# Performance work log

Hardware: AMD Instinct MI355X
Metric: run time of the kernel (lower is better)

The kernel has to match this reference:

```python
import jax, jax.numpy as jnp
import numpy as np

B, L, DM = 2, 1024, 1024
DI = 2 * DM          # expand=2
N = 16               # d_state
K = 4                # d_conv
DTR = DM // 16       # dt_rank = ceil(d_model/16) = 64
EPS = 1e-5


def setup_inputs() -> dict:
    key = jax.random.key(0)
    ks = jax.random.split(key, 8)
    s = lambda k, shape, sc=0.02: jax.random.normal(k, shape, jnp.float32) * sc
    return {
        "x": jax.random.normal(ks[0], (B, L, DM), jnp.float32),
        "ln_g": jnp.ones((DM,), jnp.float32),
        "ln_b": jnp.zeros((DM,), jnp.float32),
        "in_proj_w": s(ks[1], (2 * DI, DM)),
        "conv_w": s(ks[2], (DI, 1, K), 0.1),
        "conv_b": jnp.zeros((DI,), jnp.float32),
        "x_proj_w": s(ks[3], (DTR + 2 * N, DI)),
        "dt_proj_w": s(ks[4], (DI, DTR), 0.1),
        "dt_proj_b": s(ks[5], (DI,), 0.5),
        "A_log": jnp.log(jnp.tile(jnp.arange(1, N + 1, dtype=jnp.float32), (DI, 1))),
        "D": jnp.ones((DI,), jnp.float32),
        "out_proj_w": s(ks[6], (DM, DI)),
    }


def reference(x, ln_g, ln_b, in_proj_w, conv_w, conv_b, x_proj_w,
              dt_proj_w, dt_proj_b, A_log, D, out_proj_w):
    residual = x
    # LayerNorm
    mu = x.mean(-1, keepdims=True)
    var = ((x - mu) ** 2).mean(-1, keepdims=True)
    xn = (x - mu) * jax.lax.rsqrt(var + EPS) * ln_g + ln_b
    # in_proj -> (x, z)
    xz = jnp.einsum('bld,ed->ble', xn, in_proj_w)   # (B,L,2*DI)
    xi, z = jnp.split(xz, 2, axis=-1)
    # depthwise causal conv1d + SiLU
    xc = jax.lax.conv_general_dilated(
        xi.transpose(0, 2, 1), conv_w, (1,), [(K - 1, 0)],
        feature_group_count=DI, dimension_numbers=('NCH', 'OIH', 'NCH'))
    u = jax.nn.silu((xc + conv_b[None, :, None]).transpose(0, 2, 1))  # (B,L,DI)
    # x_proj -> dt, B, C
    xdbl = jnp.einsum('bld,ed->ble', u, x_proj_w)
    dt, Bc, Cc = jnp.split(xdbl, [DTR, DTR + N], axis=-1)
    delta = jax.nn.softplus(jnp.einsum('blr,dr->bld', dt, dt_proj_w) + dt_proj_b)
    A = -jnp.exp(A_log)                              # (DI,N)
    dA = jnp.exp(delta[..., None] * A)               # (B,L,DI,N)
    dBu = delta[..., None] * Bc[:, :, None, :] * u[..., None]

    def step(h, inp):
        dA_t, dBu_t, C_t = inp                        # (B,DI,N),(B,DI,N),(B,N)
        h = dA_t * h + dBu_t
        y = jnp.einsum('bdn,bn->bd', h, C_t)
        return h, y

    h0 = jnp.zeros((B, DI, N), x.dtype)
    _, ys = jax.lax.scan(step, h0, (dA.transpose(1, 0, 2, 3),
                                    dBu.transpose(1, 0, 2, 3),
                                    Cc.transpose(1, 0, 2)))
    y = ys.transpose(1, 0, 2) + u * D                # (B,L,DI)
    y = y * jax.nn.silu(z)
    out = jnp.einsum('bld,ed->ble', y, out_proj_w)
    return residual + out
```

## Files before the change

### kernel.cpp

```cpp
#include <hip/hip_runtime.h>
#include <hip/hip_bf16.h>
#include <math.h>

#define B_   2
#define L_   1024
#define DM_  1024
#define DI_  2048
#define NS_  16
#define DTR_ 64
#define M_   (B_ * L_)
#define XZW_ (2 * DI_)
#define XDW_ 128
#define CH_  32
#define CLEN_ (L_ / CH_)
#define SK_  8
#define KCH_ (DI_ / SK_)

typedef __attribute__((ext_vector_type(8))) short bf16x8;
typedef __attribute__((ext_vector_type(4))) float f32x4;
typedef __attribute__((ext_vector_type(4))) unsigned short u16x4;

static __device__ __forceinline__ unsigned short f2bf(float f) {
  __hip_bfloat16 h = __float2bfloat16(f);
  return *reinterpret_cast<unsigned short*>(&h);
}
static __device__ __forceinline__ float bf2f(unsigned short u) {
  unsigned int x = ((unsigned int)u) << 16;
  float f;
  __builtin_memcpy(&f, &x, 4);
  return f;
}

__global__ __launch_bounds__(256) void ln_kernel(
    const float* __restrict__ x, const float* __restrict__ g,
    const float* __restrict__ b, unsigned short* __restrict__ xnb)
{
  int r = blockIdx.x;
  int t = threadIdx.x;
  const float4* xr = (const float4*)(x + (size_t)r * DM_);
  float4 v = xr[t];
  float s  = v.x + v.y + v.z + v.w;
  float ss = v.x * v.x + v.y * v.y + v.z * v.z + v.w * v.w;
  for (int m = 32; m >= 1; m >>= 1) {
    s  += __shfl_down(s, m);
    ss += __shfl_down(ss, m);
  }
  __shared__ float sb[4], ssb[4];
  int w = t >> 6, lane = t & 63;
  if (lane == 0) { sb[w] = s; ssb[w] = ss; }
  __syncthreads();
  s  = sb[0] + sb[1] + sb[2] + sb[3];
  ss = ssb[0] + ssb[1] + ssb[2] + ssb[3];
  float mu  = s * (1.f / DM_);
  float var = ss * (1.f / DM_) - mu * mu;
  float rs  = rsqrtf(var + 1e-5f);
  float4 gv = ((const float4*)g)[t];
  float4 bv = ((const float4*)b)[t];
  u16x4 o;
  o[0] = f2bf((v.x - mu) * rs * gv.x + bv.x);
  o[1] = f2bf((v.y - mu) * rs * gv.y + bv.y);
  o[2] = f2bf((v.z - mu) * rs * gv.z + bv.z);
  o[3] = f2bf((v.w - mu) * rs * gv.w + bv.w);
  ((u16x4*)xnb)[r * 256 + t] = o;
}

__global__ __launch_bounds__(256) void f2bf_kernel(
    const float4* __restrict__ in, u16x4* __restrict__ outp)
{
  int i = blockIdx.x * 256 + threadIdx.x;
  float4 v = in[i];
  u16x4 o;
  o[0] = f2bf(v.x); o[1] = f2bf(v.y); o[2] = f2bf(v.z); o[3] = f2bf(v.w);
  outp[i] = o;
}

template<int MODE>
__global__ __launch_bounds__(256) void gemm_mfma(
    const short* __restrict__ A, int lda,
    const short* __restrict__ Bw, int ldb,
    float* __restrict__ C, int ldc, int Kdim,
    const float* __restrict__ res, int ldres)
{
  __shared__ __align__(16) short As[128 * 64];
  __shared__ __align__(16) short Bs[128 * 64];
  const int bm = blockIdx.y * 128, bn = blockIdx.x * 128;
  const int t = threadIdx.x, wid = t >> 6, lane = t & 63;
  const int wr = wid >> 1, wc = wid & 1;

  f32x4 acc[4][4];
#pragma unroll
  for (int i = 0; i < 4; ++i)
#pragma unroll
    for (int j = 0; j < 4; ++j) acc[i][j] = (f32x4){0.f, 0.f, 0.f, 0.f};

  const int srow = wid * 8 + (lane >> 3);
  const int sc   = lane & 7;
  const int r16 = lane & 15, khalf = lane >> 4;

  for (int k0 = 0; k0 < Kdim; k0 += 64) {
#pragma unroll
    for (int q = 0; q < 4; ++q) {
      int row = q * 32 + srow;
      int csw = sc ^ (row & 7);
      const short* gA = A + (size_t)(bm + row) * lda + k0 + csw * 8;
      const short* gB = Bw + (size_t)(bn + row) * ldb + k0 + csw * 8;
      __builtin_amdgcn_global_load_lds(
          (const __attribute__((address_space(1))) void*)gA,
          (__attribute__((address_space(3))) void*)(As + q * 2048 + wid * 512),
          16, 0, 0);
      __builtin_amdgcn_global_load_lds(
          (const __attribute__((address_space(1))) void*)gB,
          (__attribute__((address_space(3))) void*)(Bs + q * 2048 + wid * 512),
          16, 0, 0);
    }
    __syncthreads();

    bf16x8 af[4][2], bf[4][2];
#pragma unroll
    for (int m = 0; m < 4; ++m) {
#pragma unroll
      for (int kk = 0; kk < 2; ++kk) {
        int c16 = kk * 4 + khalf;
        int rowa = wr * 64 + m * 16 + r16;
        int rowb = wc * 64 + m * 16 + r16;
        af[m][kk] = *(const bf16x8*)(As + rowa * 64 + ((c16 ^ (rowa & 7)) << 3));
        bf[m][kk] = *(const bf16x8*)(Bs + rowb * 64 + ((c16 ^ (rowb & 7)) << 3));
      }
    }
#pragma unroll
    for (int kk = 0; kk < 2; ++kk)
#pragma unroll
      for (int m = 0; m < 4; ++m)
#pragma unroll
        for (int nn = 0; nn < 4; ++nn)
          acc[m][nn] = __builtin_amdgcn_mfma_f32_16x16x32_bf16(
              af[m][kk], bf[nn][kk], acc[m][nn], 0, 0, 0);
    __syncthreads();
  }

  const int rgrp = lane >> 4;
#pragma unroll
  for (int m = 0; m < 4; ++m)
#pragma unroll
    for (int nn = 0; nn < 4; ++nn) {
      int col = bn + wc * 64 + nn * 16 + r16;
#pragma unroll
      for (int rg = 0; rg < 4; ++rg) {
        int row = bm + wr * 64 + m * 16 + rgrp * 4 + rg;
        float v = acc[m][nn][rg];
        if (MODE == 2) v += res[(size_t)row * ldres + col];
        C[(size_t)row * ldc + col] = v;
      }
    }
}

#define BM 64
#define BN 64
#define BK 32
#define PADR 68

__global__ __launch_bounds__(256) void gemm_nt(
    const float* __restrict__ A, int lda,
    const float* __restrict__ Bw, int ldb,
    float* __restrict__ C, int ldc,
    int Mrows, int Ncols, int Kdim,
    int mode, const float* __restrict__ bias)
{
  __shared__ float as[BK][PADR];
  __shared__ float bs[BK][PADR];
  int bm = blockIdx.y * BM;
  int bn = blockIdx.x * BN;
  int t  = threadIdx.x;
  int tx = t & 15, ty = t >> 4;

  float acc[4][4] = {};

  int m0 = t >> 3;
  int kq = t & 7;
  const float4 z4 = {0.f, 0.f, 0.f, 0.f};

  for (int k0 = 0; k0 < Kdim; k0 += BK) {
    float4 a0 = *(const float4*)(A + (size_t)(bm + m0) * lda + k0 + kq * 4);
    float4 a1 = *(const float4*)(A + (size_t)(bm + m0 + 32) * lda + k0 + kq * 4);
    float4 b0 = (bn + m0 < Ncols)
        ? *(const float4*)(Bw + (size_t)(bn + m0) * ldb + k0 + kq * 4) : z4;
    float4 b1 = (bn + m0 + 32 < Ncols)
        ? *(const float4*)(Bw + (size_t)(bn + m0 + 32) * ldb + k0 + kq * 4) : z4;
    as[kq * 4 + 0][m0] = a0.x;  as[kq * 4 + 1][m0] = a0.y;
    as[kq * 4 + 2][m0] = a0.z;  as[kq * 4 + 3][m0] = a0.w;
    as[kq * 4 + 0][m0 + 32] = a1.x;  as[kq * 4 + 1][m0 + 32] = a1.y;
    as[kq * 4 + 2][m0 + 32] = a1.z;  as[kq * 4 + 3][m0 + 32] = a1.w;
    bs[kq * 4 + 0][m0] = b0.x;  bs[kq * 4 + 1][m0] = b0.y;
    bs[kq * 4 + 2][m0] = b0.z;  bs[kq * 4 + 3][m0] = b0.w;
    bs[kq * 4 + 0][m0 + 32] = b1.x;  bs[kq * 4 + 1][m0 + 32] = b1.y;
    bs[kq * 4 + 2][m0 + 32] = b1.z;  bs[kq * 4 + 3][m0 + 32] = b1.w;
    __syncthreads();

#pragma unroll
    for (int kk = 0; kk < BK; ++kk) {
      float4 a4 = *(const float4*)&as[kk][ty * 4];
      float4 b4 = *(const float4*)&bs[kk][tx * 4];
      float ar[4] = {a4.x, a4.y, a4.z, a4.w};
      float br[4] = {b4.x, b4.y, b4.z, b4.w};
#pragma unroll
      for (int i = 0; i < 4; ++i)
#pragma unroll
        for (int j = 0; j < 4; ++j)
          acc[i][j] = fmaf(ar[i], br[j], acc[i][j]);
    }
    __syncthreads();
  }

#pragma unroll
  for (int i = 0; i < 4; ++i) {
    int r = bm + ty * 4 + i;
    int c = bn + tx * 4;
    float vv[4];
#pragma unroll
    for (int j = 0; j < 4; ++j) {
      float v = acc[i][j];
      if (mode == 1) {
        v += bias[c + j];
        v = (v > 20.f) ? v : log1pf(expf(v));
      }
      vv[j] = v;
    }
    float4 o = {vv[0], vv[1], vv[2], vv[3]};
    *(float4*)(C + (size_t)r * ldc + c) = o;
  }
}

__global__ __launch_bounds__(256) void gemm_nt_sk(
    const float* __restrict__ A, int lda,
    const float* __restrict__ Bw, int ldb,
    float* __restrict__ part, int Ncols)
{
  __shared__ float as[BK][PADR];
  __shared__ float bs[BK][PADR];
  int bm = blockIdx.y * BM;
  int bn = blockIdx.x * BN;
  int sk = blockIdx.z;
  int t  = threadIdx.x;
  int tx = t & 15, ty = t >> 4;

  float acc[4][4] = {};

  int m0 = t >> 3;
  int kq = t & 7;
  const float4 z4 = {0.f, 0.f, 0.f, 0.f};

  for (int k0 = sk * KCH_; k0 < (sk + 1) * KCH_; k0 += BK) {
    float4 a0 = *(const float4*)(A + (size_t)(bm + m0) * lda + k0 + kq * 4);
    float4 a1 = *(const float4*)(A + (size_t)(bm + m0 + 32) * lda + k0 + kq * 4);
    float4 b0 = (bn + m0 < Ncols)
        ? *(const float4*)(Bw + (size_t)(bn + m0) * ldb + k0 + kq * 4) : z4;
    float4 b1 = (bn + m0 + 32 < Ncols)
        ? *(const float4*)(Bw + (size_t)(bn + m0 + 32) * ldb + k0 + kq * 4) : z4;
    as[kq * 4 + 0][m0] = a0.x;  as[kq * 4 + 1][m0] = a0.y;
    as[kq * 4 + 2][m0] = a0.z;  as[kq * 4 + 3][m0] = a0.w;
    as[kq * 4 + 0][m0 + 32] = a1.x;  as[kq * 4 + 1][m0 + 32] = a1.y;
    as[kq * 4 + 2][m0 + 32] = a1.z;  as[kq * 4 + 3][m0 + 32] = a1.w;
    bs[kq * 4 + 0][m0] = b0.x;  bs[kq * 4 + 1][m0] = b0.y;
    bs[kq * 4 + 2][m0] = b0.z;  bs[kq * 4 + 3][m0] = b0.w;
    bs[kq * 4 + 0][m0 + 32] = b1.x;  bs[kq * 4 + 1][m0 + 32] = b1.y;
    bs[kq * 4 + 2][m0 + 32] = b1.z;  bs[kq * 4 + 3][m0 + 32] = b1.w;
    __syncthreads();

#pragma unroll
    for (int kk = 0; kk < BK; ++kk) {
      float4 a4 = *(const float4*)&as[kk][ty * 4];
      float4 b4 = *(const float4*)&bs[kk][tx * 4];
      float ar[4] = {a4.x, a4.y, a4.z, a4.w};
      float br[4] = {b4.x, b4.y, b4.z, b4.w};
#pragma unroll
      for (int i = 0; i < 4; ++i)
#pragma unroll
        for (int j = 0; j < 4; ++j)
          acc[i][j] = fmaf(ar[i], br[j], acc[i][j]);
    }
    __syncthreads();
  }

  float* outp = part + (size_t)sk * M_ * XDW_;
#pragma unroll
  for (int i = 0; i < 4; ++i) {
    int r = bm + ty * 4 + i;
    int c = bn + tx * 4;
    float4 o = {acc[i][0], acc[i][1], acc[i][2], acc[i][3]};
    *(float4*)(outp + (size_t)r * XDW_ + c) = o;
  }
}

__global__ __launch_bounds__(256) void reduce_sk(
    const float* __restrict__ part, float* __restrict__ xdbl)
{
  int i = blockIdx.x * 256 + threadIdx.x;
  float s = 0.f;
#pragma unroll
  for (int sk = 0; sk < SK_; ++sk) s += part[(size_t)sk * M_ * XDW_ + i];
  xdbl[i] = s;
}

#define LCH 32
__global__ __launch_bounds__(256) void conv_silu_kernel(
    const float* __restrict__ xz, const float* __restrict__ cw,
    const float* __restrict__ cb, float* __restrict__ u)
{
  int d  = blockIdx.x * 256 + threadIdx.x;
  int l0 = blockIdx.y * LCH;
  int b  = blockIdx.z;
  float w0 = cw[d * 4 + 0], w1 = cw[d * 4 + 1];
  float w2 = cw[d * 4 + 2], w3 = cw[d * 4 + 3];
  float bias = cb[d];
  const float* xi = xz + (size_t)(b * L_) * XZW_ + d;
  float x3 = (l0 >= 3) ? xi[(size_t)(l0 - 3) * XZW_] : 0.f;
  float x2 = (l0 >= 2) ? xi[(size_t)(l0 - 2) * XZW_] : 0.f;
  float x1 = (l0 >= 1) ? xi[(size_t)(l0 - 1) * XZW_] : 0.f;
  for (int l = l0; l < l0 + LCH; ++l) {
    float x0 = xi[(size_t)l * XZW_];
    float v = w0 * x3 + w1 * x2 + w2 * x1 + w3 * x0 + bias;
    float uu = v / (1.f + __expf(-v));
    u[((size_t)(b * L_) + l) * DI_ + d] = uu;
    x3 = x2; x2 = x1; x1 = x0;
  }
}

__global__ __launch_bounds__(256) void scan_p1(
    const float* __restrict__ dlt, const float* __restrict__ u,
    const float* __restrict__ xdbl, const float* __restrict__ A_log,
    float* __restrict__ Pbuf, unsigned short* __restrict__ hend)
{
  int t = threadIdx.x;
  int ng = t & 3, dl = t >> 2;
  int d = blockIdx.x * 64 + dl;
  int b = blockIdx.y;
  int c = blockIdx.z;
  int l0 = c * CLEN_;
  float4 Al = *(const float4*)(A_log + d * NS_ + ng * 4);
  float A0 = -__expf(Al.x), A1 = -__expf(Al.y), A2 = -__expf(Al.z), A3 = -__expf(Al.w);
  float h0 = 0.f, h1 = 0.f, h2 = 0.f, h3 = 0.f, S = 0.f;
  const float* dp = dlt + ((size_t)(b * L_) + l0) * DI_ + d;
  const float* up = u   + ((size_t)(b * L_) + l0) * DI_ + d;
  const float* xp = xdbl + ((size_t)(b * L_) + l0) * XDW_ + DTR_ + ng * 4;
  float dv = dp[0], uv = up[0];
  float4 Bv = *(const float4*)xp;
  for (int l = 0; l < CLEN_; ++l) {
    int ln = (l + 1 < CLEN_) ? l + 1 : l;
    float dv_n = dp[(size_t)ln * DI_];
    float uv_n = up[(size_t)ln * DI_];
    float4 Bv_n = *(const float4*)(xp + (size_t)ln * XDW_);
    float dvu = dv * uv;
    h0 = __expf(dv * A0) * h0 + dvu * Bv.x;
    h1 = __expf(dv * A1) * h1 + dvu * Bv.y;
    h2 = __expf(dv * A2) * h2 + dvu * Bv.z;
    h3 = __expf(dv * A3) * h3 + dvu * Bv.w;
    S += dv;
    dv = dv_n; uv = uv_n; Bv = Bv_n;
  }
  size_t i = ((size_t)((b * CH_ + c) * DI_) + d) * NS_ + ng * 4;
  float4 P; P.x = __expf(S * A0); P.y = __expf(S * A1);
  P.z = __expf(S * A2); P.w = __expf(S * A3);
  u16x4 H; H[0] = f2bf(h0); H[1] = f2bf(h1); H[2] = f2bf(h2); H[3] = f2bf(h3);
  *(float4*)(Pbuf + i) = P;
  *(u16x4*)(hend + i) = H;
}

__global__ __launch_bounds__(256) void scan_p2(
    float* __restrict__ Pbuf, const unsigned short* __restrict__ hend)
{
  int tid = blockIdx.x * 256 + threadIdx.x;
  int n = tid & 15;
  int d = (tid >> 4) & (DI_ - 1);
  int b = tid >> 15;
  float h = 0.f;
  for (int c = 0; c < CH_; ++c) {
    size_t i = ((size_t)((b * CH_ + c) * DI_) + d) * NS_ + n;
    float Pv = Pbuf[i];
    float he = bf2f(hend[i]);
    Pbuf[i] = h;
    h = Pv * h + he;
  }
}

__global__ __launch_bounds__(256) void scan_p3(
    const float* __restrict__ dlt, const float* __restrict__ u,
    const float* __restrict__ xdbl, const float* __restrict__ A_log,
    const float* __restrict__ hin, const float* __restrict__ xz,
    const float* __restrict__ Dp, unsigned short* __restrict__ yb)
{
  int t = threadIdx.x;
  int ng = t & 3, dl = t >> 2;
  int d = blockIdx.x * 64 + dl;
  int b = blockIdx.y;
  int c = blockIdx.z;
  int l0 = c * CLEN_;
  float4 Al = *(const float4*)(A_log + d * NS_ + ng * 4);
  float A0 = -__expf(Al.x), A1 = -__expf(Al.y), A2 = -__expf(Al.z), A3 = -__expf(Al.w);
  size_t i0 = ((size_t)((b * CH_ + c) * DI_) + d) * NS_ + ng * 4;
  float4 hv = *(const float4*)(hin + i0);
  float h0 = hv.x, h1 = hv.y, h2 = hv.z, h3 = hv.w;
  float Dd = Dp[d];
  const float* dp = dlt + ((size_t)(b * L_) + l0) * DI_ + d;
  const float* up = u   + ((size_t)(b * L_) + l0) * DI_ + d;
  const float* xp = xdbl + ((size_t)(b * L_) + l0) * XDW_ + DTR_ + ng * 4;
  const float* zp = xz + ((size_t)(b * L_) + l0) * XZW_ + DI_ + d;
  unsigned short* yp = yb + ((size_t)(b * L_) + l0) * DI_ + d;
  float dv = dp[0], uv = up[0];
  float4 Bv = *(const float4*)xp;
  float4 Cv = *(const float4*)(xp + NS_);
  for (int l = 0; l < CLEN_; ++l) {
    int ln = (l + 1 < CLEN_) ? l + 1 : l;
    float dv_n = dp[(size_t)ln * DI_];
    float uv_n = up[(size_t)ln * DI_];
    float4 Bv_n = *(const float4*)(xp + (size_t)ln * XDW_);
    float4 Cv_n = *(const float4*)(xp + (size_t)ln * XDW_ + NS_);
    float dvu = dv * uv;
    h0 = __expf(dv * A0) * h0 + dvu * Bv.x;
    h1 = __expf(dv * A1) * h1 + dvu * Bv.y;
    h2 = __expf(dv * A2) * h2 + dvu * Bv.z;
    h3 = __expf(dv * A3) * h3 + dvu * Bv.w;
    float py = h0 * Cv.x + h1 * Cv.y + h2 * Cv.z + h3 * Cv.w;
    py += __shfl_xor(py, 1);
    py += __shfl_xor(py, 2);
    if (ng == 0) {
      float z = zp[(size_t)l * XZW_];
      float zs = z / (1.f + __expf(-z));
      yp[(size_t)l * DI_] = f2bf((py + uv * Dd) * zs);
    }
    dv = dv_n; uv = uv_n; Bv = Bv_n; Cv = Cv_n;
  }
}

extern "C" void kernel_launch(void* const* d_in, const int* in_sizes, int n_in,
                              void* d_out, int out_size, void* d_ws, size_t ws_size,
                              hipStream_t stream)
{
  const float* x         = (const float*)d_in[0];
  const float* ln_g      = (const float*)d_in[1];
  const float* ln_b      = (const float*)d_in[2];
  const float* in_proj_w = (const float*)d_in[3];
  const float* conv_w    = (const float*)d_in[4];
  const float* conv_b    = (const float*)d_in[5];
  const float* x_proj_w  = (const float*)d_in[6];
  const float* dt_proj_w = (const float*)d_in[7];
  const float* dt_proj_b = (const float*)d_in[8];
  const float* A_log     = (const float*)d_in[9];
  const float* Dp        = (const float*)d_in[10];
  const float* out_proj_w= (const float*)d_in[11];
  float* out = (float*)d_out;

  float* ws = (float*)d_ws;
  float* xz   = ws;
  float* u    = ws + 8388608;
  float* xdbl = ws + 12582912;
  float* dlt  = ws + 12845056;
  unsigned short* xnb   = (unsigned short*)(ws + 17039360);
  float* winb_f = ws + 18087936;
  unsigned short* winb  = (unsigned short*)winb_f;
  unsigned short* woutb = (unsigned short*)(ws + 20185088);
  unsigned short* yb    = (unsigned short*)(ws + 21233664);
  float* Pbuf = winb_f;
  unsigned short* hendb = xnb;

  ln_kernel<<<M_, 256, 0, stream>>>(x, ln_g, ln_b, xnb);

  f2bf_kernel<<<4096, 256, 0, stream>>>((const float4*)in_proj_w, (u16x4*)winb);
  f2bf_kernel<<<2048, 256, 0, stream>>>((const float4*)out_proj_w, (u16x4*)woutb);

  gemm_mfma<0><<<dim3(XZW_ / 128, M_ / 128), 256, 0, stream>>>(
      (const short*)xnb, DM_, (const short*)winb, DM_, xz, XZW_, DM_, nullptr, 0);

  conv_silu_kernel<<<dim3(DI_ / 256, L_ / LCH, B_), 256, 0, stream>>>(
      xz, conv_w, conv_b, u);

  gemm_nt_sk<<<dim3(XDW_ / BN, M_ / BM, SK_), 256, 0, stream>>>(
      u, DI_, x_proj_w, DI_, winb_f, 96);
  reduce_sk<<<(M_ * XDW_) / 256, 256, 0, stream>>>(winb_f, xdbl);

  gemm_nt<<<dim3(DI_ / BN, M_ / BM), 256, 0, stream>>>(
      xdbl, XDW_, dt_proj_w, DTR_, dlt, DI_, M_, DI_, DTR_, 1, dt_proj_b);

  scan_p1<<<dim3(DI_ / 64, B_, CH_), 256, 0, stream>>>(dlt, u, xdbl, A_log, Pbuf, hendb);
  scan_p2<<<(B_ * DI_ * NS_) / 256, 256, 0, stream>>>(Pbuf, hendb);
  scan_p3<<<dim3(DI_ / 64, B_, CH_), 256, 0, stream>>>(
      dlt, u, xdbl, A_log, Pbuf, xz, Dp, yb);

  gemm_mfma<2><<<dim3(DM_ / 128, M_ / 128), 256, 0, stream>>>(
      (const short*)yb, DI_, (const short*)woutb, DI_, out, DM_, DI_, x, DM_);
}
```

Measured before the change: 285.9 us.

## Double-buffer MFMA GEMM LDS tiles and use narrower N tile for out_proj

```diff
diff --git a/kernel.cpp b/kernel.cpp
--- a/kernel.cpp
+++ b/kernel.cpp
@@ -74,79 +74,100 @@
   outp[i] = o;
 }
 
-template<int MODE>
+template<int MODE, int TN>
 __global__ __launch_bounds__(256) void gemm_mfma(
     const short* __restrict__ A, int lda,
     const short* __restrict__ Bw, int ldb,
     float* __restrict__ C, int ldc, int Kdim,
     const float* __restrict__ res, int ldres)
 {
-  __shared__ __align__(16) short As[128 * 64];
-  __shared__ __align__(16) short Bs[128 * 64];
-  const int bm = blockIdx.y * 128, bn = blockIdx.x * 128;
+  constexpr int MREP = (TN == 128) ? 4 : 2;
+  constexpr int NREP = 4;
+  constexpr int WM   = (TN == 128) ? 64 : 32;
+  __shared__ __align__(16) short As[2][128 * 64];
+  __shared__ __align__(16) short Bs[2][TN * 64];
+  const int bm = blockIdx.y * 128, bn = blockIdx.x * TN;
   const int t = threadIdx.x, wid = t >> 6, lane = t & 63;
-  const int wr = wid >> 1, wc = wid & 1;
-
-  f32x4 acc[4][4];
-#pragma unroll
-  for (int i = 0; i < 4; ++i)
-#pragma unroll
-    for (int j = 0; j < 4; ++j) acc[i][j] = (f32x4){0.f, 0.f, 0.f, 0.f};
+  const int wr = (TN == 128) ? (wid >> 1) : wid;
+  const int wc = (TN == 128) ? (wid & 1) : 0;
+
+  f32x4 acc[MREP][NREP];
+#pragma unroll
+  for (int i = 0; i < MREP; ++i)
+#pragma unroll
+    for (int j = 0; j < NREP; ++j) acc[i][j] = (f32x4){0.f, 0.f, 0.f, 0.f};
 
   const int srow = wid * 8 + (lane >> 3);
   const int sc   = lane & 7;
   const int r16 = lane & 15, khalf = lane >> 4;
 
-  for (int k0 = 0; k0 < Kdim; k0 += 64) {
+  auto STAGE = [&](int buf, int k0) {
 #pragma unroll
     for (int q = 0; q < 4; ++q) {
       int row = q * 32 + srow;
       int csw = sc ^ (row & 7);
       const short* gA = A + (size_t)(bm + row) * lda + k0 + csw * 8;
+      __builtin_amdgcn_global_load_lds(
+          (const __attribute__((address_space(1))) void*)gA,
+          (__attribute__((address_space(3))) void*)(&As[buf][q * 2048 + wid * 512]),
+          16, 0, 0);
+    }
+#pragma unroll
+    for (int q = 0; q < TN / 32; ++q) {
+      int row = q * 32 + srow;
+      int csw = sc ^ (row & 7);
       const short* gB = Bw + (size_t)(bn + row) * ldb + k0 + csw * 8;
       __builtin_amdgcn_global_load_lds(
-          (const __attribute__((address_space(1))) void*)gA,
-          (__attribute__((address_space(3))) void*)(As + q * 2048 + wid * 512),
+          (const __attribute__((address_space(1))) void*)gB,
+          (__attribute__((address_space(3))) void*)(&Bs[buf][q * 2048 + wid * 512]),
           16, 0, 0);
-      __builtin_amdgcn_global_load_lds(
-          (const __attribute__((address_space(1))) void*)gB,
-          (__attribute__((address_space(3))) void*)(Bs + q * 2048 + wid * 512),
-          16, 0, 0);
-    }
+    }
+  };
+
+  const int nt = Kdim >> 6;
+  STAGE(0, 0);
+  int cur = 0;
+  for (int ti = 0; ti < nt; ++ti) {
     __syncthreads();
-
-    bf16x8 af[4][2], bf[4][2];
-#pragma unroll
-    for (int m = 0; m < 4; ++m) {
+    if (ti + 1 < nt) STAGE(cur ^ 1, (ti + 1) << 6);
+
+    bf16x8 af[MREP][2], bfr[NREP][2];
+#pragma unroll
+    for (int m = 0; m < MREP; ++m)
 #pragma unroll
       for (int kk = 0; kk < 2; ++kk) {
         int c16 = kk * 4 + khalf;
-        int rowa = wr * 64 + m * 16 + r16;
-        int rowb = wc * 64 + m * 16 + r16;
-        af[m][kk] = *(const bf16x8*)(As + rowa * 64 + ((c16 ^ (rowa & 7)) << 3));
-        bf[m][kk] = *(const bf16x8*)(Bs + rowb * 64 + ((c16 ^ (rowb & 7)) << 3));
+        int rowa = wr * WM + m * 16 + r16;
+        af[m][kk] = *(const bf16x8*)(&As[cur][rowa * 64 + ((c16 ^ (rowa & 7)) << 3)]);
       }
-    }
+#pragma unroll
+    for (int nn = 0; nn < NREP; ++nn)
+#pragma unroll
+      for (int kk = 0; kk < 2; ++kk) {
+        int c16 = kk * 4 + khalf;
+        int rowb = wc * 64 + nn * 16 + r16;
+        bfr[nn][kk] = *(const bf16x8*)(&Bs[cur][rowb * 64 + ((c16 ^ (rowb & 7)) << 3)]);
+      }
 #pragma unroll
     for (int kk = 0; kk < 2; ++kk)
 #pragma unroll
-      for (int m = 0; m < 4; ++m)
-#pragma unroll
-        for (int nn = 0; nn < 4; ++nn)
+      for (int m = 0; m < MREP; ++m)
+#pragma unroll
+        for (int nn = 0; nn < NREP; ++nn)
           acc[m][nn] = __builtin_amdgcn_mfma_f32_16x16x32_bf16(
-              af[m][kk], bf[nn][kk], acc[m][nn], 0, 0, 0);
-    __syncthreads();
+              af[m][kk], bfr[nn][kk], acc[m][nn], 0, 0, 0);
+    cur ^= 1;
   }
 
   const int rgrp = lane >> 4;
 #pragma unroll
-  for (int m = 0; m < 4; ++m)
-#pragma unroll
-    for (int nn = 0; nn < 4; ++nn) {
+  for (int m = 0; m < MREP; ++m)
+#pragma unroll
+    for (int nn = 0; nn < NREP; ++nn) {
       int col = bn + wc * 64 + nn * 16 + r16;
 #pragma unroll
       for (int rg = 0; rg < 4; ++rg) {
-        int row = bm + wr * 64 + m * 16 + rgrp * 4 + rg;
+        int row = bm + wr * WM + m * 16 + rgrp * 4 + rg;
         float v = acc[m][nn][rg];
         if (MODE == 2) v += res[(size_t)row * ldres + col];
         C[(size_t)row * ldc + col] = v;
@@ -467,7 +488,7 @@
   f2bf_kernel<<<4096, 256, 0, stream>>>((const float4*)in_proj_w, (u16x4*)winb);
   f2bf_kernel<<<2048, 256, 0, stream>>>((const float4*)out_proj_w, (u16x4*)woutb);
 
-  gemm_mfma<0><<<dim3(XZW_ / 128, M_ / 128), 256, 0, stream>>>(
+  gemm_mfma<0, 128><<<dim3(XZW_ / 128, M_ / 128), 256, 0, stream>>>(
       (const short*)xnb, DM_, (const short*)winb, DM_, xz, XZW_, DM_, nullptr, 0);
 
   conv_silu_kernel<<<dim3(DI_ / 256, L_ / LCH, B_), 256, 0, stream>>>(
@@ -485,6 +506,6 @@
   scan_p3<<<dim3(DI_ / 64, B_, CH_), 256, 0, stream>>>(
       dlt, u, xdbl, A_log, Pbuf, xz, Dp, yb);
 
-  gemm_mfma<2><<<dim3(DM_ / 128, M_ / 128), 256, 0, stream>>>(
+  gemm_mfma<2, 64><<<dim3(DM_ / 64, M_ / 128), 256, 0, stream>>>(
       (const short*)yb, DI_, (const short*)woutb, DI_, out, DM_, DI_, x, DM_);
 }
```

Result: faster. 273.3 us (-4.4%).
